# Performance work log

Measured on AMD Instinct MI355X. Metric: run time of the kernel, lower is better.

The kernel has to match this reference:

```python
import jax, jax.numpy as jnp
import numpy as np

EMBED = 512
HEADS = 8
HEAD_DIM = EMBED // HEADS
WINDOW = 256
HALF = WINDOW // 2
B, S = 2, 2048


def setup_inputs() -> dict:
    key = jax.random.key(0)
    kv, kk, kq, kw = jax.random.split(key, 4)
    return {
        "values": jax.random.normal(kv, (B, 1, S, EMBED), dtype=jnp.float32),
        "keys": jax.random.normal(kk, (B, 1, S, EMBED), dtype=jnp.float32),
        "query": jax.random.normal(kq, (B, 1, S, EMBED), dtype=jnp.float32),
        "mask": jnp.ones((B, 1, 1, S), dtype=jnp.int32),
        "fc_w": jax.random.normal(kw, (EMBED, EMBED), dtype=jnp.float32) * (1.0 / np.sqrt(EMBED)),
        "fc_b": jnp.zeros((EMBED,), dtype=jnp.float32),
    }


def reference(values, keys, query, mask, fc_w, fc_b):
    b = query.shape[0]
    s = values.shape[2]
    v = values.reshape(b, s, HEADS, HEAD_DIM)
    k = keys.reshape(b, s, HEADS, HEAD_DIM)
    q = query.reshape(b, s, HEADS, HEAD_DIM)
    scale = jnp.float32(EMBED ** 0.5)

    # global token: query 0 attends to all keys
    gq = q[:, 0:1]  # (b,1,h,d)
    ge = jnp.einsum('bqhd,bkhd->bhqk', gq, k)
    ga = jax.nn.softmax(ge / scale, axis=3)
    gout = jnp.einsum('bhqk,bkhd->bqhd', ga, v)  # (b,1,h,d)

    # sliding-window queries (positions 1..s-1, band centered at local index i)
    wq = q[:, 1:]  # (b, s-1, h, d)
    qw = s - 1
    e = jnp.einsum('bqhd,bkhd->bhqk', wq, k)  # (b,h,qw,s)
    i = jnp.arange(qw)[:, None]
    j = jnp.arange(s)[None, :]
    band = (j >= i - HALF) & (j <= i + HALF)  # (qw, s)
    # faithful to original: out-of-band energies are ZERO (not -inf)
    e = jnp.where(band[None, None], e, jnp.float32(0.0))
    e = jnp.where(mask == 0, jnp.float32(-1e20), e)
    a = jax.nn.softmax(e / scale, axis=3)
    lout = jnp.einsum('bhqk,bkhd->bqhd', a, v)  # (b,qw,h,d)

    out = jnp.concatenate([gout, lout], axis=1).reshape(b, s, HEADS * HEAD_DIM)
    return out @ fc_w.T + fc_b
```

## Files before the change

kernel.cpp:

```cpp
#include <hip/hip_runtime.h>
#include <math.h>

#define EMBED 512
#define HEADS 8
#define HDIM 64
#define SLEN 2048
#define BATCH 2
#define HALFW 128
#define NCHUNK 32
#define INV_SCALE 0.044194173824159216f

typedef short bf16x8 __attribute__((ext_vector_type(8)));
typedef short s16x4  __attribute__((ext_vector_type(4)));
typedef float f32x4  __attribute__((ext_vector_type(4)));

#define MFMA16(a, b, c) __builtin_amdgcn_mfma_f32_16x16x32_bf16(a, b, c, 0, 0, 0)

__device__ __forceinline__ short f2bf(float x) {
    union { float f; unsigned u; } v; v.f = x;
    unsigned r = v.u + 0x7FFFu + ((v.u >> 16) & 1u);
    return (short)(r >> 16);
}

__device__ __forceinline__ int lidx(int row, int seg) {
    return (((seg << 6) + (row ^ seg)) << 3);
}

__device__ __forceinline__ void gll16(const short* g, short* l) {
    __builtin_amdgcn_global_load_lds(
        (const __attribute__((address_space(1))) unsigned int*)g,
        (__attribute__((address_space(3))) unsigned int*)l, 16, 0, 0);
}

__device__ __forceinline__ void stage_chunk(const short* s0, const short* s1,
                                            short* d0, short* d1, int t) {
    int off = t * 8;
    int wb  = (t >> 6) * 512;
    gll16(s0 + off,        d0 + wb);
    gll16(s0 + 2048 + off, d0 + 2048 + wb);
    gll16(s1 + off,        d1 + wb);
    gll16(s1 + 2048 + off, d1 + 2048 + wb);
}

__device__ __forceinline__ void stage_tile(const short* s, short* d, int t) {
    int off = t * 8;
    int wb  = (t >> 6) * 512;
    gll16(s + off,        d + wb);
    gll16(s + 2048 + off, d + 2048 + wb);
}

__global__ __launch_bounds__(256) void prepass(
    const float* __restrict__ q, const float* __restrict__ k,
    const float* __restrict__ v, const int* __restrict__ mask,
    const float* __restrict__ fcw,
    short* __restrict__ Kbf, short* __restrict__ Vbf, short* __restrict__ Wbf,
    float* __restrict__ gnum_part, float* __restrict__ gden_part,
    float* __restrict__ vsum_part, float* __restrict__ nval_part) {
    int d = blockIdx.x;
    int x = d & 7, i = d >> 3;
    int hb8 = x * 2 + (i >= 68);
    int ii  = (i >= 68) ? (i - 68) : i;
    int h = hb8 & 7, b = hb8 >> 3;
    int t = threadIdx.x, w = t >> 6, l = t & 63;

    if (ii >= 64) {
        int widx = hb8 * 4 + (ii - 64);
        int nb = widx >> 3, kt = widx & 7;
        size_t base = (size_t)(nb * 8 + kt) * 4096;
        int row = t >> 3, sg = t & 7;
        #pragma unroll
        for (int p = 0; p < 2; ++p) {
            int r2 = row + p * 32;
            const float* src = fcw + (size_t)(nb * 64 + r2) * EMBED + kt * 64 + sg * 8;
            float4 f0 = *(const float4*)(src);
            float4 f1 = *(const float4*)(src + 4);
            bf16x8 o;
            o[0] = f2bf(f0.x); o[1] = f2bf(f0.y); o[2] = f2bf(f0.z); o[3] = f2bf(f0.w);
            o[4] = f2bf(f1.x); o[5] = f2bf(f1.y); o[6] = f2bf(f1.z); o[7] = f2bf(f1.w);
            *(bf16x8*)&Wbf[base + lidx(r2, sg)] = o;
        }
        return;
    }

    int ch  = ii;
    int c   = ch >> 1;
    int rof = (ch & 1) * 32;
    int j0  = ch * 32;

    __shared__ float q0s[HDIM];
    __shared__ float wls[32];
    __shared__ int   m_s[32];
    __shared__ float vbuf[32][68];
    __shared__ float red[4][HDIM];
    __shared__ float redv[4][HDIM];

    int row = t >> 3, sg = t & 7;

    const float* ksrc = k + ((size_t)b * SLEN + j0 + row) * EMBED + h * HDIM + sg * 8;
    const float* vsrc = v + ((size_t)b * SLEN + j0 + row) * EMBED + h * HDIM + sg * 8;
    float4 kf0 = *(const float4*)(ksrc);
    float4 kf1 = *(const float4*)(ksrc + 4);
    float4 vf0 = *(const float4*)(vsrc);
    float4 vf1 = *(const float4*)(vsrc + 4);

    if (t < 64) q0s[t] = q[(size_t)b * SLEN * EMBED + h * HDIM + t];
    else if (t < 96) m_s[t - 64] = mask[b * SLEN + j0 + (t - 64)];
    __syncthreads();

    size_t fragbase = ((size_t)(b * HEADS + h) * NCHUNK + c) * 4096;

    *(float4*)&vbuf[row][sg * 8]     = vf0;
    *(float4*)&vbuf[row][sg * 8 + 4] = vf1;

    {
        float dot = q0s[sg*8+0]*kf0.x + q0s[sg*8+1]*kf0.y + q0s[sg*8+2]*kf0.z + q0s[sg*8+3]*kf0.w
                  + q0s[sg*8+4]*kf1.x + q0s[sg*8+5]*kf1.y + q0s[sg*8+6]*kf1.z + q0s[sg*8+7]*kf1.w;
        dot += __shfl_xor(dot, 1, 64);
        dot += __shfl_xor(dot, 2, 64);
        dot += __shfl_xor(dot, 4, 64);
        if (sg == 0) wls[row] = __expf(dot * INV_SCALE);
        if (!m_s[row]) {
            kf0 = make_float4(0.f, 0.f, 0.f, 0.f);
            kf1 = make_float4(0.f, 0.f, 0.f, 0.f);
        }
        bf16x8 o;
        o[0] = f2bf(kf0.x); o[1] = f2bf(kf0.y); o[2] = f2bf(kf0.z); o[3] = f2bf(kf0.w);
        o[4] = f2bf(kf1.x); o[5] = f2bf(kf1.y); o[6] = f2bf(kf1.z); o[7] = f2bf(kf1.w);
        *(bf16x8*)&Kbf[fragbase + lidx(rof + row, sg)] = o;
    }
    __syncthreads();

    float num = 0.f, vs = 0.f;
    #pragma unroll
    for (int jj = 0; jj < 8; ++jj) {
        int jl = w * 8 + jj;
        float vv = vbuf[jl][l];
        num += wls[jl] * vv;
        if (m_s[jl]) vs += vv;
    }
    red[w][l] = num;
    redv[w][l] = vs;

    {
        int jseg = (ch & 1) * 4 + w;
        bf16x8 o;
        #pragma unroll
        for (int e = 0; e < 8; ++e) o[e] = f2bf(vbuf[w * 8 + e][l]);
        *(bf16x8*)&Vbf[fragbase + lidx(l, jseg)] = o;
    }
    __syncthreads();

    if (w == 0) {
        gnum_part[((size_t)(b * HEADS + h) * 64 + ch) * HDIM + l] =
            red[0][l] + red[1][l] + red[2][l] + red[3][l];
        vsum_part[((size_t)b * 64 + ch) * EMBED + h * HDIM + l] =
            redv[0][l] + redv[1][l] + redv[2][l] + redv[3][l];
    } else if (w == 1) {
        float s = (l < 32) ? wls[l] : 0.f;
        #pragma unroll
        for (int off = 32; off > 0; off >>= 1) s += __shfl_xor(s, off, 64);
        if (l == 0) gden_part[(size_t)(b * HEADS + h) * 64 + ch] = s;
    } else if (w == 2 && h == 0) {
        float cc = (l < 32 && m_s[l]) ? 1.f : 0.f;
        #pragma unroll
        for (int off = 32; off > 0; off >>= 1) cc += __shfl_xor(cc, off, 64);
        if (l == 0) nval_part[b * 64 + ch] = cc;
    }
}

__global__ __launch_bounds__(256) void windowed_attn_v11(
    const float* __restrict__ q, const float* __restrict__ k,
    const float* __restrict__ v, const int* __restrict__ mask,
    const short* __restrict__ Kbf, const short* __restrict__ Vbf,
    const float* __restrict__ gnum_part, const float* __restrict__ gden_part,
    const float* __restrict__ vsum_part, const float* __restrict__ nval_part,
    short* __restrict__ Abf) {
    int dsp = blockIdx.x;
    int wid = (dsp & 7) * 64 + (dsp >> 3);
    int tile = wid & 31, h = (wid >> 5) & 7, b = wid >> 8;
    int r0 = tile * 64;
    int t = threadIdx.x, w = t >> 6, l = t & 63;
    int lg = l >> 4, lr = l & 15;

    __shared__ __align__(16) short k_s[4][4096];
    __shared__ __align__(16) short v_s[4][4096];
    __shared__ __align__(16) short wT_s[4][16][72];
    __shared__ float rsum[64];
    __shared__ float vred[4][64];
    __shared__ float gred[4][64];
    __shared__ float nv_s, gd_s;

    size_t hb = (size_t)(b * HEADS + h) * NCHUNK;
    int bh = b * HEADS + h;

    int c0 = tile - 2; if (c0 < 0) c0 = 0;
    int c1 = tile + 2; if (c1 > NCHUNK - 1) c1 = NCHUNK - 1;

    const float* qrow = q + ((size_t)b * SLEN + r0 + w * 16 + lr) * EMBED + h * HDIM;
    float4 a0 = *(const float4*)(qrow + lg * 8);
    float4 a1 = *(const float4*)(qrow + lg * 8 + 4);
    float4 a2 = *(const float4*)(qrow + 32 + lg * 8);
    float4 a3 = *(const float4*)(qrow + 32 + lg * 8 + 4);
    float vtmp[16];
    #pragma unroll
    for (int cc = 0; cc < 16; ++cc)
        vtmp[cc] = vsum_part[((size_t)b * 64 + w * 16 + cc) * EMBED + h * HDIM + l];
    float nvt = (w == 0) ? nval_part[b * 64 + l] : 0.f;
    float gtmp[16];
    float gdt = 0.f;
    if (tile == 0) {
        #pragma unroll
        for (int cc = 0; cc < 16; ++cc)
            gtmp[cc] = gnum_part[((size_t)bh * 64 + w * 16 + cc) * HDIM + l];
        if (w == 1) gdt = gden_part[(size_t)bh * 64 + l];
    }
    __builtin_amdgcn_sched_barrier(0);

    stage_chunk(Kbf + (hb + c0) * 4096, Vbf + (hb + c0) * 4096,
                &k_s[0][0], &v_s[0][0], t);
    stage_chunk(Kbf + (hb + c0 + 1) * 4096, Vbf + (hb + c0 + 1) * 4096,
                &k_s[1][0], &v_s[1][0], t);
    stage_chunk(Kbf + (hb + c0 + 2) * 4096, Vbf + (hb + c0 + 2) * 4096,
                &k_s[2][0], &v_s[2][0], t);
    __builtin_amdgcn_sched_barrier(0);

    bf16x8 qb0, qb1;
    qb0[0] = f2bf(a0.x); qb0[1] = f2bf(a0.y); qb0[2] = f2bf(a0.z); qb0[3] = f2bf(a0.w);
    qb0[4] = f2bf(a1.x); qb0[5] = f2bf(a1.y); qb0[6] = f2bf(a1.z); qb0[7] = f2bf(a1.w);
    qb1[0] = f2bf(a2.x); qb1[1] = f2bf(a2.y); qb1[2] = f2bf(a2.z); qb1[3] = f2bf(a2.w);
    qb1[4] = f2bf(a3.x); qb1[5] = f2bf(a3.y); qb1[6] = f2bf(a3.z); qb1[7] = f2bf(a3.w);
    {
        float vp = 0.f;
        #pragma unroll
        for (int cc = 0; cc < 16; ++cc) vp += vtmp[cc];
        vred[w][l] = vp;
        if (w == 0) {
            float nvv = nvt;
            #pragma unroll
            for (int off = 32; off > 0; off >>= 1) nvv += __shfl_xor(nvv, off, 64);
            if (l == 0) nv_s = nvv;
        }
        if (tile == 0) {
            float gp = 0.f;
            #pragma unroll
            for (int cc = 0; cc < 16; ++cc) gp += gtmp[cc];
            gred[w][l] = gp;
            if (w == 1) {
                float gdd = gdt;
                #pragma unroll
                for (int off = 32; off > 0; off >>= 1) gdd += __shfl_xor(gdd, off, 64);
                if (l == 0) gd_s = gdd;
            }
        }
    }

    int center = r0 + w * 16 + lr - 1;
    int lo = center - HALFW, hi = center + HALFW;

    f32x4 pv[4];
    #pragma unroll
    for (int dt = 0; dt < 4; ++dt) pv[dt] = (f32x4){0.f, 0.f, 0.f, 0.f};
    float dacc = 0.f;

    int bi = 0;
    for (int c = c0; c <= c1; ++c) {
        int rem = c1 - c;
        if (rem >= 2)      { asm volatile("s_waitcnt vmcnt(8)" ::: "memory"); }
        else if (rem == 1) { asm volatile("s_waitcnt vmcnt(4)" ::: "memory"); }
        else               { asm volatile("s_waitcnt vmcnt(0)" ::: "memory"); }
        __syncthreads();

        int jc = c * 64;
        #pragma unroll
        for (int jt = 0; jt < 4; ++jt) {
            bf16x8 ka0 = *(const bf16x8*)&k_s[bi][lidx(jt * 16 + lr, lg)];
            bf16x8 ka1 = *(const bf16x8*)&k_s[bi][lidx(jt * 16 + lr, 4 + lg)];
            f32x4 sT = (f32x4){0.f, 0.f, 0.f, 0.f};
            sT = MFMA16(ka0, qb0, sT);
            sT = MFMA16(ka1, qb1, sT);
            int jbase = jc + jt * 16 + lg * 4;
            s16x4 wq;
            #pragma unroll
            for (int r = 0; r < 4; ++r) {
                int j = jbase + r;
                float wgt = (j >= lo && j <= hi) ? (__expf(sT[r] * INV_SCALE) - 1.f) : 0.f;
                dacc += wgt;
                wq[r] = f2bf(wgt);
            }
            *(s16x4*)&wT_s[w][lr][jt * 16 + lg * 4] = wq;
        }

        bf16x8 wa0 = *(const bf16x8*)&wT_s[w][lr][lg * 8];
        bf16x8 wa1 = *(const bf16x8*)&wT_s[w][lr][32 + lg * 8];
        #pragma unroll
        for (int dt = 0; dt < 4; ++dt) {
            bf16x8 va0 = *(const bf16x8*)&v_s[bi][lidx(dt * 16 + lr, lg)];
            bf16x8 va1 = *(const bf16x8*)&v_s[bi][lidx(dt * 16 + lr, 4 + lg)];
            pv[dt] = MFMA16(wa0, va0, pv[dt]);
            pv[dt] = MFMA16(wa1, va1, pv[dt]);
        }

        if (c + 3 <= c1) {
            int bn = (bi + 3) & 3;
            stage_chunk(Kbf + (hb + c + 3) * 4096, Vbf + (hb + c + 3) * 4096,
                        &k_s[bn][0], &v_s[bn][0], t);
        }
        bi = (bi + 1) & 3;
    }

    float wfix = 0.f;
    int jx = r0 - 129;
    if (w == 0 && jx >= 0) {
        float qv = q[((size_t)b * SLEN + r0) * EMBED + h * HDIM + l];
        float kv = k[((size_t)b * SLEN + jx) * EMBED + h * HDIM + l];
        float dd = qv * kv;
        #pragma unroll
        for (int off = 32; off > 0; off >>= 1) dd += __shfl_xor(dd, off, 64);
        if (mask[b * SLEN + jx] != 0) wfix = __expf(dd * INV_SCALE) - 1.f;
        if (lg == 0) {
            #pragma unroll
            for (int dt = 0; dt < 4; ++dt)
                pv[dt][0] += wfix * v[((size_t)b * SLEN + jx) * EMBED + h * HDIM + dt * 16 + lr];
        }
    }

    dacc += __shfl_xor(dacc, 16, 64);
    dacc += __shfl_xor(dacc, 32, 64);
    if (lg == 0) rsum[w * 16 + lr] = dacc + ((w == 0 && lr == 0) ? wfix : 0.f);
    __syncthreads();

    float nv = nv_s;
    float invden[4];
    #pragma unroll
    for (int r = 0; r < 4; ++r)
        invden[r] = 1.f / (nv + rsum[w * 16 + lg * 4 + r]);

    float* obuf = (float*)&k_s[0][0];
    #pragma unroll
    for (int dt = 0; dt < 4; ++dt) {
        int dd = dt * 16 + lr;
        float vs = vred[0][dd] + vred[1][dd] + vred[2][dd] + vred[3][dd];
        #pragma unroll
        for (int r = 0; r < 4; ++r) {
            int row_local = w * 16 + lg * 4 + r;
            float o;
            if (tile == 0 && row_local == 0)
                o = (gred[0][dd] + gred[1][dd] + gred[2][dd] + gred[3][dd]) / gd_s;
            else
                o = (pv[dt][r] + vs) * invden[r];
            obuf[row_local * 68 + dd] = o;
        }
    }
    __syncthreads();

    short* Atile = Abf + ((size_t)(b * NCHUNK + tile) * 8 + h) * 4096;
    {
        int row = t >> 3, sg = t & 7;
        #pragma unroll
        for (int p = 0; p < 2; ++p) {
            int r2 = row + p * 32;
            const float* src = &obuf[r2 * 68 + sg * 8];
            bf16x8 o8;
            #pragma unroll
            for (int e = 0; e < 8; ++e) o8[e] = f2bf(src[e]);
            *(bf16x8*)&Atile[lidx(r2, sg)] = o8;
        }
    }
}

__global__ __launch_bounds__(256) void fc_gemm_v6(
    const short* __restrict__ Abf, const short* __restrict__ Wbf,
    const float* __restrict__ bias, float* __restrict__ C) {
    int bm = blockIdx.x;
    int nb = blockIdx.y;
    int t = threadIdx.x, w = t >> 6, l = t & 63;
    int lg = l >> 4, lr = l & 15;
    int wr = w >> 1, wc = w & 1;

    __shared__ __align__(16) short a_s[8][4096];
    __shared__ __align__(16) short w_s[2][4096];

    stage_tile(Abf + (size_t)(bm * 8 + 0) * 4096, &a_s[0][0], t);
    stage_tile(Wbf + (size_t)(nb * 8 + 0) * 4096, &w_s[0][0], t);
    stage_tile(Wbf + (size_t)(nb * 8 + 1) * 4096, &w_s[1][0], t);
    #pragma unroll
    for (int kt = 1; kt < 8; ++kt)
        stage_tile(Abf + (size_t)(bm * 8 + kt) * 4096, &a_s[kt][0], t);

    f32x4 acc[2][2];
    #pragma unroll
    for (int mt = 0; mt < 2; ++mt)
        #pragma unroll
        for (int nt = 0; nt < 2; ++nt) acc[mt][nt] = (f32x4){0.f, 0.f, 0.f, 0.f};

    for (int kt = 0; kt < 8; ++kt) {
        if (kt == 0)      { asm volatile("s_waitcnt vmcnt(16)" ::: "memory"); }
        else if (kt == 1) { asm volatile("s_waitcnt vmcnt(14)" ::: "memory"); }
        else if (kt < 7)  { asm volatile("s_waitcnt vmcnt(2)"  ::: "memory"); }
        else              { asm volatile("s_waitcnt vmcnt(0)"  ::: "memory"); }
        __syncthreads();

        bf16x8 af[2][2], bf_[2][2];
        #pragma unroll
        for (int mt = 0; mt < 2; ++mt) {
            af[mt][0] = *(const bf16x8*)&a_s[kt][lidx(wr * 32 + mt * 16 + lr, lg)];
            af[mt][1] = *(const bf16x8*)&a_s[kt][lidx(wr * 32 + mt * 16 + lr, 4 + lg)];
        }
        int wbuf = kt & 1;
        #pragma unroll
        for (int nt = 0; nt < 2; ++nt) {
            bf_[nt][0] = *(const bf16x8*)&w_s[wbuf][lidx(wc * 32 + nt * 16 + lr, lg)];
            bf_[nt][1] = *(const bf16x8*)&w_s[wbuf][lidx(wc * 32 + nt * 16 + lr, 4 + lg)];
        }
        #pragma unroll
        for (int mt = 0; mt < 2; ++mt)
            #pragma unroll
            for (int nt = 0; nt < 2; ++nt) {
                acc[mt][nt] = MFMA16(af[mt][0], bf_[nt][0], acc[mt][nt]);
                acc[mt][nt] = MFMA16(af[mt][1], bf_[nt][1], acc[mt][nt]);
            }

        __syncthreads();
        if (kt + 2 <= 7)
            stage_tile(Wbf + (size_t)(nb * 8 + kt + 2) * 4096, &w_s[wbuf][0], t);
    }

    float* obuf = (float*)&a_s[0][0];
    #pragma unroll
    for (int mt = 0; mt < 2; ++mt)
        #pragma unroll
        for (int nt = 0; nt < 2; ++nt) {
            int ncol = wc * 32 + nt * 16 + lr;
            float bb = bias[nb * 64 + ncol];
            #pragma unroll
            for (int reg = 0; reg < 4; ++reg) {
                int mrow = wr * 32 + mt * 16 + lg * 4 + reg;
                obuf[mrow * 68 + ncol] = acc[mt][nt][reg] + bb;
            }
        }
    __syncthreads();

    #pragma unroll
    for (int i = 0; i < 4; ++i) {
        int row = i * 16 + (t >> 4);
        int col = (t & 15) * 4;
        float4 o4 = *(const float4*)&obuf[row * 68 + col];
        *(float4*)&C[(size_t)(bm * 64 + row) * 512 + nb * 64 + col] = o4;
    }
}

extern "C" void kernel_launch(void* const* d_in, const int* in_sizes, int n_in,
                              void* d_out, int out_size, void* d_ws, size_t ws_size,
                              hipStream_t stream) {
    const float* values = (const float*)d_in[0];
    const float* keys   = (const float*)d_in[1];
    const float* query  = (const float*)d_in[2];
    const int*   maskp  = (const int*)d_in[3];
    const float* fc_w   = (const float*)d_in[4];
    const float* fc_b   = (const float*)d_in[5];
    float* out = (float*)d_out;

    short* Abf = (short*)d_ws;
    short* Wbf = Abf + (size_t)BATCH * SLEN * EMBED;
    short* Kbf = Wbf + (size_t)EMBED * EMBED;
    short* Vbf = Kbf + (size_t)BATCH * HEADS * NCHUNK * 4096;
    float* vsum_part = (float*)(Vbf + (size_t)BATCH * HEADS * NCHUNK * 4096);
    float* gnum_part = vsum_part + (size_t)BATCH * 64 * EMBED;
    float* gden_part = gnum_part + (size_t)BATCH * HEADS * 64 * HDIM;
    float* nval_part = gden_part + (size_t)BATCH * HEADS * 64;

    prepass<<<dim3(1088), 256, 0, stream>>>(
        query, keys, values, maskp, fc_w, Kbf, Vbf, Wbf,
        gnum_part, gden_part, vsum_part, nval_part);
    windowed_attn_v11<<<dim3(512), 256, 0, stream>>>(
        query, keys, values, maskp, Kbf, Vbf,
        gnum_part, gden_part, vsum_part, nval_part, Abf);
    fc_gemm_v6<<<dim3(64, 8), 256, 0, stream>>>(
        Abf, Wbf, fc_b, out);
}
```

Before: 31.09 us.

## Double attention query tile per block to share K/V chunk staging across eight waves

The windowed attention kernel now processes 128 query rows per block with 512 threads (8 waves), down from 64 rows with 256 threads. The grid shrinks to 256 blocks, and each block stages a wider chunk range once so all eight waves reuse it, which cuts redundant K/V loads from overlapping windows. Each staging call now issues half as many loads per thread, so the vmcnt waits are adjusted to match. The separate fix-up for the leftmost band-edge key is removed because that key now falls inside the staged chunk range. The trade-off is fewer blocks for occupancy and larger per-block shared-memory reductions.

```diff
diff --git a/kernel.cpp b/kernel.cpp
--- a/kernel.cpp
+++ b/kernel.cpp
@@ -32,21 +32,19 @@
         (__attribute__((address_space(3))) unsigned int*)l, 16, 0, 0);
 }
 
-__device__ __forceinline__ void stage_chunk(const short* s0, const short* s1,
-                                            short* d0, short* d1, int t) {
-    int off = t * 8;
-    int wb  = (t >> 6) * 512;
-    gll16(s0 + off,        d0 + wb);
-    gll16(s0 + 2048 + off, d0 + 2048 + wb);
-    gll16(s1 + off,        d1 + wb);
-    gll16(s1 + 2048 + off, d1 + 2048 + wb);
-}
-
 __device__ __forceinline__ void stage_tile(const short* s, short* d, int t) {
     int off = t * 8;
     int wb  = (t >> 6) * 512;
     gll16(s + off,        d + wb);
     gll16(s + 2048 + off, d + 2048 + wb);
+}
+
+__device__ __forceinline__ void stage_chunk512(const short* s0, const short* s1,
+                                               short* d0, short* d1, int t) {
+    int off = t * 8;
+    int wb  = (t >> 6) * 512;
+    gll16(s0 + off, d0 + wb);
+    gll16(s1 + off, d1 + wb);
 }
 
 __global__ __launch_bounds__(256) void prepass(
@@ -168,60 +166,60 @@
     }
 }
 
-__global__ __launch_bounds__(256) void windowed_attn_v11(
-    const float* __restrict__ q, const float* __restrict__ k,
-    const float* __restrict__ v, const int* __restrict__ mask,
+__global__ __launch_bounds__(512) void windowed_attn_v12(
+    const float* __restrict__ q,
     const short* __restrict__ Kbf, const short* __restrict__ Vbf,
     const float* __restrict__ gnum_part, const float* __restrict__ gden_part,
     const float* __restrict__ vsum_part, const float* __restrict__ nval_part,
     short* __restrict__ Abf) {
     int dsp = blockIdx.x;
-    int wid = (dsp & 7) * 64 + (dsp >> 3);
-    int tile = wid & 31, h = (wid >> 5) & 7, b = wid >> 8;
-    int r0 = tile * 64;
+    int x = dsp & 7, i = dsp >> 3;
+    int hb8 = x * 2 + (i >= 16);
+    int tlw = i & 15;
+    int h = hb8 & 7, b = hb8 >> 3;
+    int r0 = tlw * 128;
     int t = threadIdx.x, w = t >> 6, l = t & 63;
     int lg = l >> 4, lr = l & 15;
 
-    __shared__ __align__(16) short k_s[4][4096];
-    __shared__ __align__(16) short v_s[4][4096];
-    __shared__ __align__(16) short wT_s[4][16][72];
-    __shared__ float rsum[64];
-    __shared__ float vred[4][64];
-    __shared__ float gred[4][64];
+    __shared__ __align__(16) short kv_s[2][4][4096];
+    __shared__ __align__(16) short wT_s[8][16][72];
+    __shared__ float rsum[128];
+    __shared__ float vred[8][64];
+    __shared__ float gred[8][64];
     __shared__ float nv_s, gd_s;
 
     size_t hb = (size_t)(b * HEADS + h) * NCHUNK;
     int bh = b * HEADS + h;
 
-    int c0 = tile - 2; if (c0 < 0) c0 = 0;
-    int c1 = tile + 2; if (c1 > NCHUNK - 1) c1 = NCHUNK - 1;
+    int c0 = (r0 - 129) >> 6; if (c0 < 0) c0 = 0;
+    int c1 = (r0 + 254) >> 6; if (c1 > NCHUNK - 1) c1 = NCHUNK - 1;
 
     const float* qrow = q + ((size_t)b * SLEN + r0 + w * 16 + lr) * EMBED + h * HDIM;
     float4 a0 = *(const float4*)(qrow + lg * 8);
     float4 a1 = *(const float4*)(qrow + lg * 8 + 4);
     float4 a2 = *(const float4*)(qrow + 32 + lg * 8);
     float4 a3 = *(const float4*)(qrow + 32 + lg * 8 + 4);
-    float vtmp[16];
-    #pragma unroll
-    for (int cc = 0; cc < 16; ++cc)
-        vtmp[cc] = vsum_part[((size_t)b * 64 + w * 16 + cc) * EMBED + h * HDIM + l];
+    float vtmp[8];
+    #pragma unroll
+    for (int cc = 0; cc < 8; ++cc)
+        vtmp[cc] = vsum_part[((size_t)b * 64 + w * 8 + cc) * EMBED + h * HDIM + l];
     float nvt = (w == 0) ? nval_part[b * 64 + l] : 0.f;
-    float gtmp[16];
+    float gtmp[8];
     float gdt = 0.f;
-    if (tile == 0) {
-        #pragma unroll
-        for (int cc = 0; cc < 16; ++cc)
-            gtmp[cc] = gnum_part[((size_t)bh * 64 + w * 16 + cc) * HDIM + l];
+    if (tlw == 0) {
+        #pragma unroll
+        for (int cc = 0; cc < 8; ++cc)
+            gtmp[cc] = gnum_part[((size_t)bh * 64 + w * 8 + cc) * HDIM + l];
         if (w == 1) gdt = gden_part[(size_t)bh * 64 + l];
     }
     __builtin_amdgcn_sched_barrier(0);
 
-    stage_chunk(Kbf + (hb + c0) * 4096, Vbf + (hb + c0) * 4096,
-                &k_s[0][0], &v_s[0][0], t);
-    stage_chunk(Kbf + (hb + c0 + 1) * 4096, Vbf + (hb + c0 + 1) * 4096,
-                &k_s[1][0], &v_s[1][0], t);
-    stage_chunk(Kbf + (hb + c0 + 2) * 4096, Vbf + (hb + c0 + 2) * 4096,
-                &k_s[2][0], &v_s[2][0], t);
+    stage_chunk512(Kbf + (hb + c0) * 4096, Vbf + (hb + c0) * 4096,
+                   &kv_s[0][0][0], &kv_s[1][0][0], t);
+    stage_chunk512(Kbf + (hb + c0 + 1) * 4096, Vbf + (hb + c0 + 1) * 4096,
+                   &kv_s[0][1][0], &kv_s[1][1][0], t);
+    stage_chunk512(Kbf + (hb + c0 + 2) * 4096, Vbf + (hb + c0 + 2) * 4096,
+                   &kv_s[0][2][0], &kv_s[1][2][0], t);
     __builtin_amdgcn_sched_barrier(0);
 
     bf16x8 qb0, qb1;
@@ -232,7 +230,7 @@
     {
         float vp = 0.f;
         #pragma unroll
-        for (int cc = 0; cc < 16; ++cc) vp += vtmp[cc];
+        for (int cc = 0; cc < 8; ++cc) vp += vtmp[cc];
         vred[w][l] = vp;
         if (w == 0) {
             float nvv = nvt;
@@ -240,10 +238,10 @@
             for (int off = 32; off > 0; off >>= 1) nvv += __shfl_xor(nvv, off, 64);
             if (l == 0) nv_s = nvv;
         }
-        if (tile == 0) {
+        if (tlw == 0) {
             float gp = 0.f;
             #pragma unroll
-            for (int cc = 0; cc < 16; ++cc) gp += gtmp[cc];
+            for (int cc = 0; cc < 8; ++cc) gp += gtmp[cc];
             gred[w][l] = gp;
             if (w == 1) {
                 float gdd = gdt;
@@ -265,16 +263,16 @@
     int bi = 0;
     for (int c = c0; c <= c1; ++c) {
         int rem = c1 - c;
-        if (rem >= 2)      { asm volatile("s_waitcnt vmcnt(8)" ::: "memory"); }
-        else if (rem == 1) { asm volatile("s_waitcnt vmcnt(4)" ::: "memory"); }
+        if (rem >= 2)      { asm volatile("s_waitcnt vmcnt(4)" ::: "memory"); }
+        else if (rem == 1) { asm volatile("s_waitcnt vmcnt(2)" ::: "memory"); }
         else               { asm volatile("s_waitcnt vmcnt(0)" ::: "memory"); }
         __syncthreads();
 
         int jc = c * 64;
         #pragma unroll
         for (int jt = 0; jt < 4; ++jt) {
-            bf16x8 ka0 = *(const bf16x8*)&k_s[bi][lidx(jt * 16 + lr, lg)];
-            bf16x8 ka1 = *(const bf16x8*)&k_s[bi][lidx(jt * 16 + lr, 4 + lg)];
+            bf16x8 ka0 = *(const bf16x8*)&kv_s[0][bi][lidx(jt * 16 + lr, lg)];
+            bf16x8 ka1 = *(const bf16x8*)&kv_s[0][bi][lidx(jt * 16 + lr, 4 + lg)];
             f32x4 sT = (f32x4){0.f, 0.f, 0.f, 0.f};
             sT = MFMA16(ka0, qb0, sT);
             sT = MFMA16(ka1, qb1, sT);
@@ -294,39 +292,23 @@
         bf16x8 wa1 = *(const bf16x8*)&wT_s[w][lr][32 + lg * 8];
         #pragma unroll
         for (int dt = 0; dt < 4; ++dt) {
-            bf16x8 va0 = *(const bf16x8*)&v_s[bi][lidx(dt * 16 + lr, lg)];
-            bf16x8 va1 = *(const bf16x8*)&v_s[bi][lidx(dt * 16 + lr, 4 + lg)];
+            bf16x8 va0 = *(const bf16x8*)&kv_s[1][bi][lidx(dt * 16 + lr, lg)];
+            bf16x8 va1 = *(const bf16x8*)&kv_s[1][bi][lidx(dt * 16 + lr, 4 + lg)];
             pv[dt] = MFMA16(wa0, va0, pv[dt]);
             pv[dt] = MFMA16(wa1, va1, pv[dt]);
         }
 
         if (c + 3 <= c1) {
             int bn = (bi + 3) & 3;
-            stage_chunk(Kbf + (hb + c + 3) * 4096, Vbf + (hb + c + 3) * 4096,
-                        &k_s[bn][0], &v_s[bn][0], t);
+            stage_chunk512(Kbf + (hb + c + 3) * 4096, Vbf + (hb + c + 3) * 4096,
+                           &kv_s[0][bn][0], &kv_s[1][bn][0], t);
         }
         bi = (bi + 1) & 3;
-    }
-
-    float wfix = 0.f;
-    int jx = r0 - 129;
-    if (w == 0 && jx >= 0) {
-        float qv = q[((size_t)b * SLEN + r0) * EMBED + h * HDIM + l];
-        float kv = k[((size_t)b * SLEN + jx) * EMBED + h * HDIM + l];
-        float dd = qv * kv;
-        #pragma unroll
-        for (int off = 32; off > 0; off >>= 1) dd += __shfl_xor(dd, off, 64);
-        if (mask[b * SLEN + jx] != 0) wfix = __expf(dd * INV_SCALE) - 1.f;
-        if (lg == 0) {
-            #pragma unroll
-            for (int dt = 0; dt < 4; ++dt)
-                pv[dt][0] += wfix * v[((size_t)b * SLEN + jx) * EMBED + h * HDIM + dt * 16 + lr];
-        }
     }
 
     dacc += __shfl_xor(dacc, 16, 64);
     dacc += __shfl_xor(dacc, 32, 64);
-    if (lg == 0) rsum[w * 16 + lr] = dacc + ((w == 0 && lr == 0) ? wfix : 0.f);
+    if (lg == 0) rsum[w * 16 + lr] = dacc;
     __syncthreads();
 
     float nv = nv_s;
@@ -335,17 +317,20 @@
     for (int r = 0; r < 4; ++r)
         invden[r] = 1.f / (nv + rsum[w * 16 + lg * 4 + r]);
 
-    float* obuf = (float*)&k_s[0][0];
+    float* obuf = (float*)&kv_s[0][0][0];
     #pragma unroll
     for (int dt = 0; dt < 4; ++dt) {
         int dd = dt * 16 + lr;
-        float vs = vred[0][dd] + vred[1][dd] + vred[2][dd] + vred[3][dd];
+        float vs = 0.f;
+        #pragma unroll
+        for (int ww = 0; ww < 8; ++ww) vs += vred[ww][dd];
         #pragma unroll
         for (int r = 0; r < 4; ++r) {
             int row_local = w * 16 + lg * 4 + r;
             float o;
-            if (tile == 0 && row_local == 0)
-                o = (gred[0][dd] + gred[1][dd] + gred[2][dd] + gred[3][dd]) / gd_s;
+            if (tlw == 0 && row_local == 0)
+                o = (gred[0][dd] + gred[1][dd] + gred[2][dd] + gred[3][dd] +
+                     gred[4][dd] + gred[5][dd] + gred[6][dd] + gred[7][dd]) / gd_s;
             else
                 o = (pv[dt][r] + vs) * invden[r];
             obuf[row_local * 68 + dd] = o;
@@ -353,17 +338,17 @@
     }
     __syncthreads();
 
-    short* Atile = Abf + ((size_t)(b * NCHUNK + tile) * 8 + h) * 4096;
     {
         int row = t >> 3, sg = t & 7;
         #pragma unroll
         for (int p = 0; p < 2; ++p) {
-            int r2 = row + p * 32;
+            int r2 = row + p * 64;
+            short* Atile = Abf + ((size_t)(b * NCHUNK + tlw * 2 + (r2 >> 6)) * 8 + h) * 4096;
             const float* src = &obuf[r2 * 68 + sg * 8];
             bf16x8 o8;
             #pragma unroll
             for (int e = 0; e < 8; ++e) o8[e] = f2bf(src[e]);
-            *(bf16x8*)&Atile[lidx(r2, sg)] = o8;
+            *(bf16x8*)&Atile[lidx(r2 & 63, sg)] = o8;
         }
     }
 }
@@ -472,8 +457,8 @@
     prepass<<<dim3(1088), 256, 0, stream>>>(
         query, keys, values, maskp, fc_w, Kbf, Vbf, Wbf,
         gnum_part, gden_part, vsum_part, nval_part);
-    windowed_attn_v11<<<dim3(512), 256, 0, stream>>>(
-        query, keys, values, maskp, Kbf, Vbf,
+    windowed_attn_v12<<<dim3(256), 512, 0, stream>>>(
+        query, Kbf, Vbf,
         gnum_part, gden_part, vsum_part, nval_part, Abf);
     fc_gemm_v6<<<dim3(64, 8), 256, 0, stream>>>(
         Abf, Wbf, fc_b, out);
```

Measured after the change: 32.07 us. 1.03x slower.
